# Performance work log

Hardware: AMD Instinct MI355X
Metric: run time of the kernel (lower is better)

## Reference

```python
import jax, jax.numpy as jnp
import numpy as np
import math

B, S, T = 64, 512, 512
N, F_NODE, F_TRIP = 2000, 128, 128
D, H, GD = 512, 8, 64  # concat fusion: D == H*GD
SECONDS_PER_DAY = 3600.0 * 24.0


def cyclical_feat(t, mask):
    # t,[B,L]; mask,[B,L] -> [B,L,2]  (matches tf concat of sin/cos on axis 2)
    ang = 2.0 * math.pi * t / SECONDS_PER_DAY
    return jnp.stack([jnp.sin(ang) * mask, jnp.cos(ang) * mask], axis=-1)


def gat(x, adj, W, a_src, a_dst):
    # GAT-style AttentionAggregator, concat fusion + relu activation.
    # x:[N,F], adj:[N,N] (0/1), W:[H,F,G], a_src/a_dst:[H,G]
    h = jnp.einsum('nf,hfg->hng', x, W)                      # [H,N,G]
    es = jnp.einsum('hng,hg->hn', h, a_src)                  # [H,N]
    ed = jnp.einsum('hng,hg->hn', h, a_dst)                  # [H,N]
    e = jax.nn.leaky_relu(es[:, :, None] + ed[:, None, :], 0.2)  # [H,N,N]
    e = jnp.where(adj[None, :, :] > 0, e, -1e9)
    attn = jax.nn.softmax(e, axis=-1)                        # [H,N,N]
    out = jnp.einsum('hij,hjg->hig', attn, h)                # [H,N,G]
    out = jnp.transpose(out, (1, 0, 2)).reshape(x.shape[0], -1)  # [N,H*G]
    return jax.nn.relu(out)


def reconstruct_from_graph(graph_emb, index_array):
    # Vectorized equivalent of the TF TensorArray loop: indices are 1-based
    # with 0 = pad; valid entries are left-compacted, so masked gather == 
    # boolean_mask + gather + right-pad.
    valid = index_array > 0                                   # [B,S]
    idx = jnp.maximum(index_array - 1, 0)                     # [B,S]
    return jnp.where(valid[..., None], graph_emb[idx], 0.0)   # [B,S,D]


def setup_inputs() -> dict:
    key = jax.random.key(0)
    ks = jax.random.split(key, 13)
    region_batch = jax.random.normal(ks[0], (N, F_NODE), jnp.float32)
    trip_batch = jax.random.normal(ks[1], (B, T, F_TRIP), jnp.float32)
    len_r = jax.random.randint(ks[2], (B,), S // 2, S + 1)
    len_t = jax.random.randint(ks[3], (B,), T // 2, T + 1)
    region_mask = (jnp.arange(S)[None, :] < len_r[:, None]).astype(jnp.float32)
    trip_mask = (jnp.arange(T)[None, :] < len_t[:, None]).astype(jnp.float32)
    graph_mask = (jax.random.uniform(ks[4], (N, N)) < 0.02).astype(jnp.float32)
    graph_mask = jnp.maximum(graph_mask, jnp.eye(N, dtype=jnp.float32))  # self loops
    index_array = jax.random.randint(ks[5], (B, S), 1, N + 1).astype(jnp.int32)
    index_array = index_array * region_mask.astype(jnp.int32)  # 0 = pad (right side)
    arrive = jax.random.uniform(ks[6], (B, S), jnp.float32, 0.0, SECONDS_PER_DAY)
    depart = jax.random.uniform(ks[7], (B, T), jnp.float32, 0.0, SECONDS_PER_DAY)
    W_trip = jax.random.normal(ks[8], (F_TRIP, D), jnp.float32) * 0.05
    W_gat = jax.random.normal(ks[9], (H, F_NODE, GD), jnp.float32) * 0.05
    a_src = jax.random.normal(ks[10], (H, GD), jnp.float32) * 0.05
    a_dst = jax.random.normal(ks[11], (H, GD), jnp.float32) * 0.05
    W_time = jax.random.normal(ks[12], (2, D), jnp.float32) * 0.05
    b_time = jnp.zeros((D,), jnp.float32)
    return dict(region_batch=region_batch, trip_batch=trip_batch,
                trip_mask=trip_mask, region_mask=region_mask, graph_mask=graph_mask,
                arrive=arrive, depart=depart, index_array=index_array,
                W_trip=W_trip, W_gat=W_gat, a_src=a_src, a_dst=a_dst,
                W_time=W_time, b_time=b_time)


def reference(region_batch, trip_batch, trip_mask, region_mask, graph_mask,
              arrive, depart, index_array, W_trip, W_gat, a_src, a_dst,
              W_time, b_time):
    # FeatureExtractionLayer assumed Dense(no bias) + relu; dropout=0 (eval).
    trip_embeddings = jax.nn.relu(jnp.einsum('btf,fd->btd', trip_batch, W_trip))
    graph_embeddings = gat(region_batch, graph_mask, W_gat, a_src, a_dst)  # [N,D]
    region_embeddings = reconstruct_from_graph(graph_embeddings, index_array)
    arrive_feat = cyclical_feat(arrive, region_mask)   # [B,S,2]
    depart_feat = cyclical_feat(depart, trip_mask)     # [B,T,2]
    region_embeddings = region_embeddings + arrive_feat @ W_time + b_time
    trip_embeddings = trip_embeddings + depart_feat @ W_time + b_time
    return (region_embeddings, trip_embeddings)
```

## Files before the change

### kernel.cpp

```cpp
#include <hip/hip_runtime.h>
#include <hip/hip_bf16.h>

#define NB 2000
#define FN 128
#define DD 512
#define HH 8
#define GG 64
#define BB 64
#define SS 512
#define TT 512

__device__ __forceinline__ bool is_bf16(const void* graph_mask) {
    return (((const unsigned*)graph_mask)[0] & 0xFFFFu) == 0x3F80u;
}

template<bool BF>
__device__ __forceinline__ float ld(const void* p, long i) {
    if constexpr (BF) return __bfloat162float(((const __hip_bfloat16*)p)[i]);
    else              return ((const float*)p)[i];
}
template<bool BF>
__device__ __forceinline__ void st(void* p, long i, float v) {
    if constexpr (BF) ((__hip_bfloat16*)p)[i] = __float2bfloat16(v);
    else              ((float*)p)[i] = v;
}

template<bool BF>
__device__ __forceinline__ void ld4(const void* p, long i, float* o) {
    if constexpr (BF) {
        const unsigned short* q = (const unsigned short*)p + i;
        uint2 v = *reinterpret_cast<const uint2*>(q);
        o[0] = __uint_as_float((v.x & 0xFFFFu) << 16);
        o[1] = __uint_as_float((v.x >> 16) << 16);
        o[2] = __uint_as_float((v.y & 0xFFFFu) << 16);
        o[3] = __uint_as_float((v.y >> 16) << 16);
    } else {
        float4 a = *reinterpret_cast<const float4*>((const float*)p + i);
        o[0]=a.x; o[1]=a.y; o[2]=a.z; o[3]=a.w;
    }
}
template<bool BF>
__device__ __forceinline__ void ld8(const void* p, long i, float* o) {
    if constexpr (BF) {
        const unsigned short* q = (const unsigned short*)p + i;
        uint4 v = *reinterpret_cast<const uint4*>(q);
        unsigned a0 = v.x, a1 = v.y, a2 = v.z, a3 = v.w;
        o[0] = __uint_as_float((a0 & 0xFFFFu) << 16);
        o[1] = __uint_as_float((a0 >> 16) << 16);
        o[2] = __uint_as_float((a1 & 0xFFFFu) << 16);
        o[3] = __uint_as_float((a1 >> 16) << 16);
        o[4] = __uint_as_float((a2 & 0xFFFFu) << 16);
        o[5] = __uint_as_float((a2 >> 16) << 16);
        o[6] = __uint_as_float((a3 & 0xFFFFu) << 16);
        o[7] = __uint_as_float((a3 >> 16) << 16);
    } else {
        const float* q = (const float*)p + i;
        float4 a = *reinterpret_cast<const float4*>(q);
        float4 b = *reinterpret_cast<const float4*>(q + 4);
        o[0]=a.x; o[1]=a.y; o[2]=a.z; o[3]=a.w;
        o[4]=b.x; o[5]=b.y; o[6]=b.z; o[7]=b.w;
    }
}
__device__ __forceinline__ unsigned pack_bf2(float a, float b) {
    __hip_bfloat16 x = __float2bfloat16(a), y = __float2bfloat16(b);
    return (unsigned)*(unsigned short*)&x | ((unsigned)*(unsigned short*)&y << 16);
}
template<bool BF>
__device__ __forceinline__ void st8(void* p, long i, const float* v) {
    if constexpr (BF) {
        unsigned short* q = (unsigned short*)p + i;
        *reinterpret_cast<uint4*>(q) = make_uint4(
            pack_bf2(v[0], v[1]), pack_bf2(v[2], v[3]),
            pack_bf2(v[4], v[5]), pack_bf2(v[6], v[7]));
    } else {
        float* q = (float*)p + i;
        *reinterpret_cast<float4*>(q)     = make_float4(v[0],v[1],v[2],v[3]);
        *reinterpret_cast<float4*>(q + 4) = make_float4(v[4],v[5],v[6],v[7]);
    }
}

__device__ __forceinline__ unsigned short f2bf(float v) {
    __hip_bfloat16 h = __float2bfloat16(v);
    return *reinterpret_cast<unsigned short*>(&h);
}
__device__ __forceinline__ float bf2f(unsigned short s) {
    return __uint_as_float((unsigned)s << 16);
}

#define NPB 8

template<bool BF>
__device__ __forceinline__ void gat_h_body(
    const void* __restrict__ x, const void* __restrict__ Wg,
    const void* __restrict__ a_src, const void* __restrict__ a_dst,
    float* __restrict__ h_ws, float* __restrict__ es_ws, float* __restrict__ ed_ws,
    float (*__restrict__ xs)[FN])
{
    int n0  = blockIdx.x * NPB;
    int tid = threadIdx.x;
    int hh  = tid >> 5, gp = tid & 31;
    int g0  = gp * 2;

    if constexpr (BF) {
        for (int idx = tid; idx < NPB * FN / 8; idx += 256) {
            float o[8];
            ld8<BF>(x, (long)n0 * FN + idx * 8, o);
#pragma unroll
            for (int j = 0; j < 8; ++j) ((float*)xs)[idx * 8 + j] = o[j];
        }
    } else {
        const float4* src = (const float4*)((const float*)x + (long)n0 * FN);
        for (int idx = tid; idx < NPB * FN / 4; idx += 256)
            ((float4*)xs)[idx] = src[idx];
    }
    __syncthreads();

    float v0[NPB], v1[NPB];
#pragma unroll
    for (int nn = 0; nn < NPB; ++nn) { v0[nn] = 0.f; v1[nn] = 0.f; }

    if constexpr (BF) {
        const unsigned* wp = (const unsigned*)((const unsigned short*)Wg + (long)hh * FN * GG);
#pragma unroll 4
        for (int f = 0; f < FN; ++f) {
            unsigned w = wp[f * 32 + gp];
            float wx = __uint_as_float((w & 0xFFFFu) << 16);
            float wy = __uint_as_float((w >> 16) << 16);
#pragma unroll
            for (int nn = 0; nn < NPB; ++nn) {
                float xf = xs[nn][f];
                v0[nn] = fmaf(xf, wx, v0[nn]);
                v1[nn] = fmaf(xf, wy, v1[nn]);
            }
        }
    } else {
        const float2* wp = (const float2*)((const float*)Wg + (long)hh * FN * GG);
#pragma unroll 4
        for (int f = 0; f < FN; ++f) {
            float2 w = wp[f * 32 + gp];
#pragma unroll
            for (int nn = 0; nn < NPB; ++nn) {
                float xf = xs[nn][f];
                v0[nn] = fmaf(xf, w.x, v0[nn]);
                v1[nn] = fmaf(xf, w.y, v1[nn]);
            }
        }
    }

    float as0 = ld<BF>(a_src, hh * GG + g0), as1 = ld<BF>(a_src, hh * GG + g0 + 1);
    float ad0 = ld<BF>(a_dst, hh * GG + g0), ad1 = ld<BF>(a_dst, hh * GG + g0 + 1);
#pragma unroll
    for (int nn = 0; nn < NPB; ++nn) {
        int n = n0 + nn;
        *reinterpret_cast<float2*>(&h_ws[((long)hh * NB + n) * GG + g0]) =
            make_float2(v0[nn], v1[nn]);
        float s1 = v0[nn] * as0 + v1[nn] * as1;
        float s2 = v0[nn] * ad0 + v1[nn] * ad1;
        for (int off = 16; off > 0; off >>= 1) {
            s1 += __shfl_xor(s1, off);
            s2 += __shfl_xor(s2, off);
        }
        if (gp == 0) { es_ws[hh * NB + n] = s1; ed_ws[hh * NB + n] = s2; }
    }
}

__global__ __launch_bounds__(256) void gat_h_kernel(
    const void* x, const void* Wg, const void* a_src, const void* a_dst,
    float* h_ws, float* es_ws, float* ed_ws, const void* graph_mask)
{
    __shared__ float xs[NPB][FN];
    if (is_bf16(graph_mask)) gat_h_body<true >(x, Wg, a_src, a_dst, h_ws, es_ws, ed_ws, xs);
    else                     gat_h_body<false>(x, Wg, a_src, a_dst, h_ws, es_ws, ed_ws, xs);
}

#define ACAP 192

template<bool BF>
__device__ __forceinline__ void gat_attn_body(
    const void* __restrict__ adj,
    const float* __restrict__ h_ws, const float* __restrict__ es_ws,
    const float* __restrict__ ed_ws, float* __restrict__ ge_ws,
    int* __restrict__ jl, float (*__restrict__ wts)[ACAP],
    float* __restrict__ es_i, int* __restrict__ cnt)
{
    const int i    = blockIdx.x;
    const int tid  = threadIdx.x;
    const int w    = tid >> 6;
    const int lane = tid & 63;

    if (tid == 0) *cnt = 0;
    if (tid < HH) es_i[tid] = es_ws[tid * NB + i];
    __syncthreads();

    for (int base = w * 64; base < NB; base += 512) {
        int  j     = base + lane;
        bool valid = (j < NB) && (ld<BF>(adj, (long)i * NB + j) > 0.f);
        unsigned long long mask = __ballot(valid);
        int nv = __popcll(mask);
        int bs = 0;
        if (lane == 0 && nv) bs = atomicAdd(cnt, nv);
        bs = __shfl(bs, 0);
        if (valid) {
            int slot = bs + __popcll(mask & ((1ULL << lane) - 1ULL));
            jl[slot] = j;
        }
    }
    __syncthreads();
    const int cn = min(*cnt, ACAP);

    const float es = es_i[w];
    float e_r[3];
    float m = -INFINITY;
#pragma unroll
    for (int s = 0; s < 3; ++s) {
        int k = lane + s * 64;
        float e = -INFINITY;
        if (k < cn) {
            float ev = es + ed_ws[(long)w * NB + jl[k]];
            e = ev > 0.f ? ev : 0.2f * ev;
        }
        e_r[s] = e;
        m = fmaxf(m, e);
    }
    for (int off = 32; off > 0; off >>= 1) m = fmaxf(m, __shfl_xor(m, off));
    float l = 0.f;
#pragma unroll
    for (int s = 0; s < 3; ++s) {
        int k = lane + s * 64;
        if (k < cn) {
            float p = __expf(e_r[s] - m);
            wts[w][k] = p;
            l += p;
        }
    }
    for (int off = 32; off > 0; off >>= 1) l += __shfl_xor(l, off);

    const float* hp = h_ws + (long)w * NB * GG + lane;
    float acc = 0.f;
    int k = 0;
    for (; k + 4 <= cn; k += 4) {
        float e0 = wts[w][k],   e1 = wts[w][k+1];
        float e2 = wts[w][k+2], e3 = wts[w][k+3];
        int   j0 = jl[k],   j1 = jl[k+1], j2 = jl[k+2], j3 = jl[k+3];
        float h0 = hp[(long)j0 * GG];
        float h1 = hp[(long)j1 * GG];
        float h2 = hp[(long)j2 * GG];
        float h3 = hp[(long)j3 * GG];
        acc = fmaf(e3, h3, fmaf(e2, h2, fmaf(e1, h1, fmaf(e0, h0, acc))));
    }
    for (; k < cn; ++k)
        acc = fmaf(wts[w][k], hp[(long)jl[k] * GG], acc);

    ge_ws[(long)i * DD + w * GG + lane] = fmaxf(acc / l, 0.f);
}

__global__ __launch_bounds__(512) void gat_attn_kernel(
    const void* adj, const float* h_ws, const float* es_ws,
    const float* ed_ws, float* ge_ws)
{
    __shared__ int   jl[2048];
    __shared__ float wts[HH][ACAP];
    __shared__ float es_i[HH];
    __shared__ int   cnt;
    if (is_bf16(adj)) gat_attn_body<true >(adj, h_ws, es_ws, ed_ws, ge_ws, jl, wts, es_i, &cnt);
    else              gat_attn_body<false>(adj, h_ws, es_ws, ed_ws, ge_ws, jl, wts, es_i, &cnt);
}

template<bool BF>
__device__ __forceinline__ void region_out_body(
    const int* __restrict__ index_array, const void* __restrict__ arrive,
    const void* __restrict__ region_mask,
    const void* __restrict__ W_time, const void* __restrict__ b_time,
    const float* __restrict__ ge_ws, void* __restrict__ out)
{
    int row  = blockIdx.x * 4 + (threadIdx.x >> 6);
    int lane = threadIdx.x & 63;
    int d0   = lane * 8;
    int idx  = index_array[row];
    float mask = ld<BF>(region_mask, row);
    float t    = ld<BF>(arrive, row);
    float ang  = 6.28318530717958647692f * t / 86400.f;
    float sa = sinf(ang) * mask, ca = cosf(ang) * mask;
    float g[8] = {0.f,0.f,0.f,0.f,0.f,0.f,0.f,0.f};
    if (idx > 0) {
        const float* gp = ge_ws + (long)(idx - 1) * DD + d0;
        float4 a = *reinterpret_cast<const float4*>(gp);
        float4 b = *reinterpret_cast<const float4*>(gp + 4);
        g[0]=a.x; g[1]=a.y; g[2]=a.z; g[3]=a.w;
        g[4]=b.x; g[5]=b.y; g[6]=b.z; g[7]=b.w;
    }
    float wt0[8], wt1[8], bt[8], o[8];
    ld8<BF>(W_time, d0, wt0);
    ld8<BF>(W_time, DD + d0, wt1);
    ld8<BF>(b_time, d0, bt);
#pragma unroll
    for (int j = 0; j < 8; ++j)
        o[j] = g[j] + sa * wt0[j] + ca * wt1[j] + bt[j];
    st8<BF>(out, (long)row * DD + d0, o);
}

__global__ __launch_bounds__(256) void region_out_kernel(
    const int* index_array, const void* arrive, const void* region_mask,
    const void* W_time, const void* b_time, const float* ge_ws, void* out,
    const void* graph_mask)
{
    if (is_bf16(graph_mask))
        region_out_body<true >(index_array, arrive, region_mask, W_time, b_time, ge_ws, out);
    else
        region_out_body<false>(index_array, arrive, region_mask, W_time, b_time, ge_ws, out);
}

typedef __attribute__((ext_vector_type(8))) short bf16x8;
typedef __attribute__((ext_vector_type(4))) float f32x4;

#define MFMA_BF16 __builtin_amdgcn_mfma_f32_16x16x32_bf16

template<bool BF>
__device__ __forceinline__ void trip_mfma_body(
    const void* __restrict__ trip_batch, const void* __restrict__ W_trip,
    const void* __restrict__ depart, const void* __restrict__ trip_mask,
    const void* __restrict__ W_time, const void* __restrict__ b_time,
    void* __restrict__ out,
    short* __restrict__ Xh, short* __restrict__ Xl,
    short* __restrict__ Wh, short* __restrict__ Wl)
{
    const int tid  = threadIdx.x;
    const int lane = tid & 63;
    const int wv   = tid >> 6;
    const int bx   = blockIdx.x & 7;
    const int by   = blockIdx.x >> 3;
    const int row0 = by * 64;
    const int c0   = bx * 64;

    f32x4 acc0 = {0.f,0.f,0.f,0.f}, acc1 = {0.f,0.f,0.f,0.f};
    f32x4 acc2 = {0.f,0.f,0.f,0.f}, acc3 = {0.f,0.f,0.f,0.f};

    const int mr  = wv * 16 + (lane & 15);
    const int nrb = lane & 15;
    const int kl  = (lane >> 4) * 8;

    for (int kh = 0; kh < 2; ++kh) {
        if (kh) __syncthreads();

        for (int q = tid; q < 1024; q += 256) {
            int r  = q >> 4;
            int k4 = (q & 15) * 4;
            float v[4];
            ld4<BF>(trip_batch, (long)(row0 + r) * FN + kh * 64 + k4, v);
            int base = r * 64 + (k4 ^ ((r & 7) << 3));
            ushort4 hs, ls;
            hs.x = f2bf(v[0]); ls.x = f2bf(v[0] - bf2f(hs.x));
            hs.y = f2bf(v[1]); ls.y = f2bf(v[1] - bf2f(hs.y));
            hs.z = f2bf(v[2]); ls.z = f2bf(v[2] - bf2f(hs.z));
            hs.w = f2bf(v[3]); ls.w = f2bf(v[3] - bf2f(hs.w));
            *reinterpret_cast<ushort4*>(&Xh[base]) = hs;
            *reinterpret_cast<ushort4*>(&Xl[base]) = ls;
        }
        for (int q = tid; q < 1024; q += 256) {
            int k  = q >> 4;
            int n0 = (q & 15) * 4;
            float v[4];
            ld4<BF>(W_trip, (long)(kh * 64 + k) * DD + c0 + n0, v);
#pragma unroll
            for (int j = 0; j < 4; ++j) {
                int n   = n0 + j;
                int idx = n * 64 + (k ^ ((n & 7) << 3));
                unsigned short h = f2bf(v[j]);
                Wh[idx] = (short)h;
                Wl[idx] = (short)f2bf(v[j] - bf2f(h));
            }
        }
        __syncthreads();

#pragma unroll
        for (int kc = 0; kc < 2; ++kc) {
            int k0 = kc * 32 + kl;
            int ax = mr * 64 + (k0 ^ ((mr & 7) << 3));
            bf16x8 ah = *reinterpret_cast<const bf16x8*>(&Xh[ax]);
            bf16x8 al = *reinterpret_cast<const bf16x8*>(&Xl[ax]);
            {
                int nr = 0 + nrb, wi = nr * 64 + (k0 ^ ((nr & 7) << 3));
                bf16x8 bh = *reinterpret_cast<const bf16x8*>(&Wh[wi]);
                bf16x8 bl = *reinterpret_cast<const bf16x8*>(&Wl[wi]);
                acc0 = MFMA_BF16(ah, bh, acc0, 0, 0, 0);
                acc0 = MFMA_BF16(al, bh, acc0, 0, 0, 0);
                acc0 = MFMA_BF16(ah, bl, acc0, 0, 0, 0);
            }
            {
                int nr = 16 + nrb, wi = nr * 64 + (k0 ^ ((nr & 7) << 3));
                bf16x8 bh = *reinterpret_cast<const bf16x8*>(&Wh[wi]);
                bf16x8 bl = *reinterpret_cast<const bf16x8*>(&Wl[wi]);
                acc1 = MFMA_BF16(ah, bh, acc1, 0, 0, 0);
                acc1 = MFMA_BF16(al, bh, acc1, 0, 0, 0);
                acc1 = MFMA_BF16(ah, bl, acc1, 0, 0, 0);
            }
            {
                int nr = 32 + nrb, wi = nr * 64 + (k0 ^ ((nr & 7) << 3));
                bf16x8 bh = *reinterpret_cast<const bf16x8*>(&Wh[wi]);
                bf16x8 bl = *reinterpret_cast<const bf16x8*>(&Wl[wi]);
                acc2 = MFMA_BF16(ah, bh, acc2, 0, 0, 0);
                acc2 = MFMA_BF16(al, bh, acc2, 0, 0, 0);
                acc2 = MFMA_BF16(ah, bl, acc2, 0, 0, 0);
            }
            {
                int nr = 48 + nrb, wi = nr * 64 + (k0 ^ ((nr & 7) << 3));
                bf16x8 bh = *reinterpret_cast<const bf16x8*>(&Wh[wi]);
                bf16x8 bl = *reinterpret_cast<const bf16x8*>(&Wl[wi]);
                acc3 = MFMA_BF16(ah, bh, acc3, 0, 0, 0);
                acc3 = MFMA_BF16(al, bh, acc3, 0, 0, 0);
                acc3 = MFMA_BF16(ah, bl, acc3, 0, 0, 0);
            }
        }
    }

    const int rbase = row0 + wv * 16 + (lane >> 4) * 4;
    float sa[4], ca[4];
#pragma unroll
    for (int r = 0; r < 4; ++r) {
        int   row  = rbase + r;
        float mask = ld<BF>(trip_mask, row);
        float t    = ld<BF>(depart, row);
        float ang  = 6.28318530717958647692f * t / 86400.f;
        sa[r] = sinf(ang) * mask;
        ca[r] = cosf(ang) * mask;
    }
    const long obase = (long)BB * SS * DD;
#pragma unroll
    for (int nt = 0; nt < 4; ++nt) {
        int   c   = c0 + nt * 16 + (lane & 15);
        float wt0 = ld<BF>(W_time, c);
        float wt1 = ld<BF>(W_time, DD + c);
        float bt  = ld<BF>(b_time, c);
        f32x4 a = (nt == 0) ? acc0 : (nt == 1) ? acc1 : (nt == 2) ? acc2 : acc3;
#pragma unroll
        for (int r = 0; r < 4; ++r) {
            float o = fmaxf(a[r], 0.f) + sa[r] * wt0 + ca[r] * wt1 + bt;
            st<BF>(out, obase + (long)(rbase + r) * DD + c, o);
        }
    }
}

__global__ __launch_bounds__(256) void trip_out_kernel(
    const void* trip_batch, const void* W_trip, const void* depart,
    const void* trip_mask, const void* W_time, const void* b_time, void* out,
    const void* graph_mask)
{
    __shared__ short Xh[64 * 64], Xl[64 * 64];
    __shared__ short Wh[64 * 64], Wl[64 * 64];
    if (is_bf16(graph_mask))
        trip_mfma_body<true >(trip_batch, W_trip, depart, trip_mask, W_time, b_time, out, Xh, Xl, Wh, Wl);
    else
        trip_mfma_body<false>(trip_batch, W_trip, depart, trip_mask, W_time, b_time, out, Xh, Xl, Wh, Wl);
}

extern "C" void kernel_launch(void* const* d_in, const int* in_sizes, int n_in,
                              void* d_out, int out_size, void* d_ws, size_t ws_size,
                              hipStream_t stream) {
    const void* region_batch = d_in[0];
    const void* trip_batch   = d_in[1];
    const void* trip_mask    = d_in[2];
    const void* region_mask  = d_in[3];
    const void* graph_mask   = d_in[4];
    const void* arrive       = d_in[5];
    const void* depart       = d_in[6];
    const int*  index_array  = (const int*)d_in[7];
    const void* W_trip       = d_in[8];
    const void* W_gat        = d_in[9];
    const void* a_src        = d_in[10];
    const void* a_dst        = d_in[11];
    const void* W_time       = d_in[12];
    const void* b_time       = d_in[13];

    float* h_ws  = (float*)d_ws;
    float* es_ws = h_ws  + HH * NB * GG;
    float* ed_ws = es_ws + HH * NB;
    float* ge_ws = ed_ws + HH * NB;

    gat_h_kernel<<<NB / NPB, 256, 0, stream>>>(region_batch, W_gat, a_src, a_dst,
                                               h_ws, es_ws, ed_ws, graph_mask);
    gat_attn_kernel<<<NB, 512, 0, stream>>>(graph_mask, h_ws, es_ws, ed_ws, ge_ws);
    region_out_kernel<<<BB * SS / 4, 256, 0, stream>>>(index_array, arrive, region_mask,
                                                       W_time, b_time, ge_ws, d_out, graph_mask);
    trip_out_kernel<<<(BB * TT / 64) * (DD / 64), 256, 0, stream>>>(
        trip_batch, W_trip, depart, trip_mask, W_time, b_time, d_out, graph_mask);
}
```

Baseline: 286.3 us.

## Precompute bf16 hi/lo splits of trip inputs and weights in prep kernels

Adds two prep kernels that convert trip_batch and W_trip once into bf16 high/low halves. The weights are stored transposed so the GEMM can load them with 16-byte copies. The new trip GEMM kernel then copies these pre-split tiles into shared memory instead of converting fp32 in every tile block, and it skips the low-half MFMAs when inputs are bf16. This removes redundant per-block conversion, since W was re-split by every row block. In exchange it adds two extra launches and a workspace round trip of about 16 MB of split activations.

```diff
diff --git a/kernel.cpp b/kernel.cpp
--- a/kernel.cpp
+++ b/kernel.cpp
@@ -315,6 +315,171 @@
 
 #define MFMA_BF16 __builtin_amdgcn_mfma_f32_16x16x32_bf16
 
+__global__ __launch_bounds__(256) void prep_x_kernel(
+    const void* __restrict__ trip_batch, unsigned short* __restrict__ Xh_p,
+    unsigned short* __restrict__ Xl_p, const void* graph_mask)
+{
+    if (is_bf16(graph_mask)) return;
+    long i = ((long)blockIdx.x * 256 + threadIdx.x) * 8;
+    const float* q = (const float*)trip_batch + i;
+    float4 a = *reinterpret_cast<const float4*>(q);
+    float4 b = *reinterpret_cast<const float4*>(q + 4);
+    float v[8] = {a.x,a.y,a.z,a.w,b.x,b.y,b.z,b.w};
+    unsigned short h[8], l[8];
+#pragma unroll
+    for (int j = 0; j < 8; ++j) {
+        h[j] = f2bf(v[j]);
+        l[j] = f2bf(v[j] - bf2f(h[j]));
+    }
+    *reinterpret_cast<uint4*>(Xh_p + i) = make_uint4(
+        h[0] | ((unsigned)h[1] << 16), h[2] | ((unsigned)h[3] << 16),
+        h[4] | ((unsigned)h[5] << 16), h[6] | ((unsigned)h[7] << 16));
+    *reinterpret_cast<uint4*>(Xl_p + i) = make_uint4(
+        l[0] | ((unsigned)l[1] << 16), l[2] | ((unsigned)l[3] << 16),
+        l[4] | ((unsigned)l[5] << 16), l[6] | ((unsigned)l[7] << 16));
+}
+
+__global__ __launch_bounds__(256) void prep_w_kernel(
+    const void* __restrict__ W_trip, unsigned short* __restrict__ Wh_p,
+    unsigned short* __restrict__ Wl_p, const void* graph_mask)
+{
+    bool bf = is_bf16(graph_mask);
+    int q  = blockIdx.x * 256 + threadIdx.x;
+    int k  = q >> 7;
+    int n0 = (q & 127) * 4;
+    if (bf) {
+        const unsigned short* w = (const unsigned short*)W_trip;
+#pragma unroll
+        for (int j = 0; j < 4; ++j)
+            Wh_p[(n0 + j) * FN + k] = w[(long)k * DD + n0 + j];
+    } else {
+        float v[4];
+        ld4<false>(W_trip, (long)k * DD + n0, v);
+#pragma unroll
+        for (int j = 0; j < 4; ++j) {
+            unsigned short h = f2bf(v[j]);
+            Wh_p[(n0 + j) * FN + k] = h;
+            Wl_p[(n0 + j) * FN + k] = f2bf(v[j] - bf2f(h));
+        }
+    }
+}
+
+template<bool BF>
+__device__ __forceinline__ void trip_gemm_body(
+    const unsigned short* __restrict__ Xh_p, const unsigned short* __restrict__ Xl_p,
+    const unsigned short* __restrict__ Wh_p, const unsigned short* __restrict__ Wl_p,
+    const void* __restrict__ depart, const void* __restrict__ trip_mask,
+    const void* __restrict__ W_time, const void* __restrict__ b_time,
+    void* __restrict__ out,
+    short* __restrict__ Xh, short* __restrict__ Xl,
+    short* __restrict__ Wh, short* __restrict__ Wl)
+{
+    const int tid  = threadIdx.x;
+    const int lane = tid & 63;
+    const int wv   = tid >> 6;
+    const int bx   = blockIdx.x & 7;
+    const int by   = blockIdx.x >> 3;
+    const int row0 = by * 64;
+    const int c0   = bx * 64;
+
+    f32x4 acc0 = {0.f,0.f,0.f,0.f}, acc1 = {0.f,0.f,0.f,0.f};
+    f32x4 acc2 = {0.f,0.f,0.f,0.f}, acc3 = {0.f,0.f,0.f,0.f};
+
+    const int mr  = wv * 16 + (lane & 15);
+    const int nrb = lane & 15;
+    const int kl  = (lane >> 4) * 8;
+
+    for (int kh = 0; kh < 2; ++kh) {
+        if (kh) __syncthreads();
+
+        for (int q = tid; q < 512; q += 256) {
+            int r  = q >> 3, k8 = q & 7;
+            long src = (long)(row0 + r) * FN + kh * 64 + k8 * 8;
+            int  dst = r * 64 + ((k8 * 8) ^ ((r & 7) << 3));
+            *reinterpret_cast<uint4*>(&Xh[dst]) =
+                *reinterpret_cast<const uint4*>(Xh_p + src);
+            if constexpr (!BF)
+                *reinterpret_cast<uint4*>(&Xl[dst]) =
+                    *reinterpret_cast<const uint4*>(Xl_p + src);
+        }
+        for (int q = tid; q < 512; q += 256) {
+            int n  = q >> 3, k8 = q & 7;
+            long src = (long)(c0 + n) * FN + kh * 64 + k8 * 8;
+            int  dst = n * 64 + ((k8 * 8) ^ ((n & 7) << 3));
+            *reinterpret_cast<uint4*>(&Wh[dst]) =
+                *reinterpret_cast<const uint4*>(Wh_p + src);
+            if constexpr (!BF)
+                *reinterpret_cast<uint4*>(&Wl[dst]) =
+                    *reinterpret_cast<const uint4*>(Wl_p + src);
+        }
+        __syncthreads();
+
+#pragma unroll
+        for (int kc = 0; kc < 2; ++kc) {
+            int k0 = kc * 32 + kl;
+            int ax = mr * 64 + (k0 ^ ((mr & 7) << 3));
+            bf16x8 ah = *reinterpret_cast<const bf16x8*>(&Xh[ax]);
+            bf16x8 al;
+            if constexpr (!BF) al = *reinterpret_cast<const bf16x8*>(&Xl[ax]);
+#pragma unroll
+            for (int nt = 0; nt < 4; ++nt) {
+                int nr = nt * 16 + nrb, wi = nr * 64 + (k0 ^ ((nr & 7) << 3));
+                bf16x8 bh = *reinterpret_cast<const bf16x8*>(&Wh[wi]);
+                f32x4& acc = (nt == 0) ? acc0 : (nt == 1) ? acc1 : (nt == 2) ? acc2 : acc3;
+                acc = MFMA_BF16(ah, bh, acc, 0, 0, 0);
+                if constexpr (!BF) {
+                    bf16x8 bl = *reinterpret_cast<const bf16x8*>(&Wl[wi]);
+                    acc = MFMA_BF16(al, bh, acc, 0, 0, 0);
+                    acc = MFMA_BF16(ah, bl, acc, 0, 0, 0);
+                }
+            }
+        }
+    }
+
+    const int rbase = row0 + wv * 16 + (lane >> 4) * 4;
+    float sa[4], ca[4];
+#pragma unroll
+    for (int r = 0; r < 4; ++r) {
+        int   row  = rbase + r;
+        float mask = ld<BF>(trip_mask, row);
+        float t    = ld<BF>(depart, row);
+        float ang  = 6.28318530717958647692f * t / 86400.f;
+        sa[r] = sinf(ang) * mask;
+        ca[r] = cosf(ang) * mask;
+    }
+    const long obase = (long)BB * SS * DD;
+#pragma unroll
+    for (int nt = 0; nt < 4; ++nt) {
+        int   c   = c0 + nt * 16 + (lane & 15);
+        float wt0 = ld<BF>(W_time, c);
+        float wt1 = ld<BF>(W_time, DD + c);
+        float bt  = ld<BF>(b_time, c);
+        f32x4 a = (nt == 0) ? acc0 : (nt == 1) ? acc1 : (nt == 2) ? acc2 : acc3;
+#pragma unroll
+        for (int r = 0; r < 4; ++r) {
+            float o = fmaxf(a[r], 0.f) + sa[r] * wt0 + ca[r] * wt1 + bt;
+            st<BF>(out, obase + (long)(rbase + r) * DD + c, o);
+        }
+    }
+}
+
+__global__ __launch_bounds__(256) void trip_gemm_kernel(
+    const void* trip_batch,
+    const unsigned short* Xh_p, const unsigned short* Xl_p,
+    const unsigned short* Wh_p, const unsigned short* Wl_p,
+    const void* depart, const void* trip_mask,
+    const void* W_time, const void* b_time, void* out, const void* graph_mask)
+{
+    __shared__ short Xh[64 * 64], Xl[64 * 64];
+    __shared__ short Wh[64 * 64], Wl[64 * 64];
+    if (is_bf16(graph_mask))
+        trip_gemm_body<true >((const unsigned short*)trip_batch, Xl_p, Wh_p, Wl_p,
+                              depart, trip_mask, W_time, b_time, out, Xh, Xl, Wh, Wl);
+    else
+        trip_gemm_body<false>(Xh_p, Xl_p, Wh_p, Wl_p,
+                              depart, trip_mask, W_time, b_time, out, Xh, Xl, Wh, Wl);
+}
+
 template<bool BF>
 __device__ __forceinline__ void trip_mfma_body(
     const void* __restrict__ trip_batch, const void* __restrict__ W_trip,
@@ -341,7 +506,6 @@
 
     for (int kh = 0; kh < 2; ++kh) {
         if (kh) __syncthreads();
-
         for (int q = tid; q < 1024; q += 256) {
             int r  = q >> 4;
             int k4 = (q & 15) * 4;
@@ -378,37 +542,15 @@
             int ax = mr * 64 + (k0 ^ ((mr & 7) << 3));
             bf16x8 ah = *reinterpret_cast<const bf16x8*>(&Xh[ax]);
             bf16x8 al = *reinterpret_cast<const bf16x8*>(&Xl[ax]);
-            {
-                int nr = 0 + nrb, wi = nr * 64 + (k0 ^ ((nr & 7) << 3));
+#pragma unroll
+            for (int nt = 0; nt < 4; ++nt) {
+                int nr = nt * 16 + nrb, wi = nr * 64 + (k0 ^ ((nr & 7) << 3));
                 bf16x8 bh = *reinterpret_cast<const bf16x8*>(&Wh[wi]);
                 bf16x8 bl = *reinterpret_cast<const bf16x8*>(&Wl[wi]);
-                acc0 = MFMA_BF16(ah, bh, acc0, 0, 0, 0);
-                acc0 = MFMA_BF16(al, bh, acc0, 0, 0, 0);
-                acc0 = MFMA_BF16(ah, bl, acc0, 0, 0, 0);
-            }
-            {
-                int nr = 16 + nrb, wi = nr * 64 + (k0 ^ ((nr & 7) << 3));
-                bf16x8 bh = *reinterpret_cast<const bf16x8*>(&Wh[wi]);
-                bf16x8 bl = *reinterpret_cast<const bf16x8*>(&Wl[wi]);
-                acc1 = MFMA_BF16(ah, bh, acc1, 0, 0, 0);
-                acc1 = MFMA_BF16(al, bh, acc1, 0, 0, 0);
-                acc1 = MFMA_BF16(ah, bl, acc1, 0, 0, 0);
-            }
-            {
-                int nr = 32 + nrb, wi = nr * 64 + (k0 ^ ((nr & 7) << 3));
-                bf16x8 bh = *reinterpret_cast<const bf16x8*>(&Wh[wi]);
-                bf16x8 bl = *reinterpret_cast<const bf16x8*>(&Wl[wi]);
-                acc2 = MFMA_BF16(ah, bh, acc2, 0, 0, 0);
-                acc2 = MFMA_BF16(al, bh, acc2, 0, 0, 0);
-                acc2 = MFMA_BF16(ah, bl, acc2, 0, 0, 0);
-            }
-            {
-                int nr = 48 + nrb, wi = nr * 64 + (k0 ^ ((nr & 7) << 3));
-                bf16x8 bh = *reinterpret_cast<const bf16x8*>(&Wh[wi]);
-                bf16x8 bl = *reinterpret_cast<const bf16x8*>(&Wl[wi]);
-                acc3 = MFMA_BF16(ah, bh, acc3, 0, 0, 0);
-                acc3 = MFMA_BF16(al, bh, acc3, 0, 0, 0);
-                acc3 = MFMA_BF16(ah, bl, acc3, 0, 0, 0);
+                f32x4& acc = (nt == 0) ? acc0 : (nt == 1) ? acc1 : (nt == 2) ? acc2 : acc3;
+                acc = MFMA_BF16(ah, bh, acc, 0, 0, 0);
+                acc = MFMA_BF16(al, bh, acc, 0, 0, 0);
+                acc = MFMA_BF16(ah, bl, acc, 0, 0, 0);
             }
         }
     }
@@ -475,12 +617,27 @@
     float* es_ws = h_ws  + HH * NB * GG;
     float* ed_ws = es_ws + HH * NB;
     float* ge_ws = ed_ws + HH * NB;
+    unsigned short* Xh_p = (unsigned short*)(ge_ws + (long)NB * DD);
+    unsigned short* Xl_p = Xh_p + (long)BB * TT * FN;
+    unsigned short* Wh_p = Xl_p + (long)BB * TT * FN;
+    unsigned short* Wl_p = Wh_p + FN * DD;
+    const size_t need = (size_t)((Wl_p + FN * DD) - (unsigned short*)d_ws) * 2;
 
     gat_h_kernel<<<NB / NPB, 256, 0, stream>>>(region_batch, W_gat, a_src, a_dst,
                                                h_ws, es_ws, ed_ws, graph_mask);
     gat_attn_kernel<<<NB, 512, 0, stream>>>(graph_mask, h_ws, es_ws, ed_ws, ge_ws);
     region_out_kernel<<<BB * SS / 4, 256, 0, stream>>>(index_array, arrive, region_mask,
                                                        W_time, b_time, ge_ws, d_out, graph_mask);
-    trip_out_kernel<<<(BB * TT / 64) * (DD / 64), 256, 0, stream>>>(
-        trip_batch, W_trip, depart, trip_mask, W_time, b_time, d_out, graph_mask);
-}
+    if (ws_size >= need) {
+        prep_x_kernel<<<(BB * TT * FN) / (256 * 8), 256, 0, stream>>>(
+            trip_batch, Xh_p, Xl_p, graph_mask);
+        prep_w_kernel<<<(FN * DD / 4) / 256, 256, 0, stream>>>(
+            W_trip, Wh_p, Wl_p, graph_mask);
+        trip_gemm_kernel<<<(BB * TT / 64) * (DD / 64), 256, 0, stream>>>(
+            trip_batch, Xh_p, Xl_p, Wh_p, Wl_p,
+            depart, trip_mask, W_time, b_time, d_out, graph_mask);
+    } else {
+        trip_out_kernel<<<(BB * TT / 64) * (DD / 64), 256, 0, stream>>>(
+            trip_batch, W_trip, depart, trip_mask, W_time, b_time, d_out, graph_mask);
+    }
+}
```

Result: faster. 269.8 us (-5.8%).
